# Kernel tuning notes

Measured on AMD Instinct MI355X. Metric: run time of the kernel, lower is better.

Reference implementation:

```python
import jax, jax.numpy as jnp
import numpy as np

B, L, D, H, NH, NL = 256, 201, 1536, 64, 2, 2
FF = 4 * H  # gnn hidden = hidden_units*4, ffn hidden = 4*d_model


def setup_inputs() -> dict:
    key = jax.random.key(0)
    ks = jax.random.split(key, 16)
    def nrm(k, shp, s=0.02):
        return jax.random.normal(k, shp, jnp.float32) * s
    return dict(
        interaction_list=jax.random.normal(ks[0], (B, L, D), jnp.float32),
        neg_list=jax.random.normal(ks[1], (B, L, D), jnp.float32),
        fc_w=nrm(ks[2], (D, H)), fc_b=jnp.zeros((H,), jnp.float32),
        mlp_w=nrm(ks[3], (H, H)), mlp_b=jnp.zeros((H,), jnp.float32),
        pos_emb=nrm(ks[4], (L, H)),
        ln0_g=jnp.ones((H,), jnp.float32), ln0_b=jnp.zeros((H,), jnp.float32),
        wqkv=nrm(ks[5], (NL, H, 3 * H)), bqkv=jnp.zeros((NL, 3 * H), jnp.float32),
        wo=nrm(ks[6], (NL, H, H)), bo=jnp.zeros((NL, H), jnp.float32),
        ln1_g=jnp.ones((NL, H), jnp.float32), ln1_b=jnp.zeros((NL, H), jnp.float32),
        w1=nrm(ks[7], (NL, H, FF)), b1=jnp.zeros((NL, FF), jnp.float32),
        w2=nrm(ks[8], (NL, FF, H)), b2=jnp.zeros((NL, H), jnp.float32),
        ln2_g=jnp.ones((NL, H), jnp.float32), ln2_b=jnp.zeros((NL, H), jnp.float32),
        wg1=nrm(ks[9], (D, FF)), bg1=jnp.zeros((FF,), jnp.float32),
        wg2=nrm(ks[10], (FF, H)), bg2=jnp.zeros((H,), jnp.float32),
        interaction_mask=jax.random.randint(ks[11], (B, L), 0, 2, jnp.int32),
    )


def _ln(x, g, b, eps=1e-5):
    m = x.mean(-1, keepdims=True)
    v = ((x - m) ** 2).mean(-1, keepdims=True)
    return (x - m) / jnp.sqrt(v + eps) * g + b


def _mlp_fc(x, fc_w, fc_b, mlp_w, mlp_b):
    # MLP_Layers: Linear(LLM_size->h) then dnn_layer x [Linear(h,h)+GELU]
    x = x @ fc_w + fc_b
    return jax.nn.gelu(x @ mlp_w + mlp_b)


def _user_encoder(x, mask_f, pos_emb, ln0_g, ln0_b, wqkv, bqkv, wo, bo,
                  ln1_g, ln1_b, w1, b1, w2, b2, ln2_g, ln2_b):
    b, l, h = x.shape
    dh = h // NH
    # causal AND key-valid attention bias: tril of (log_mask != 0) over keys
    causal = jnp.tril(jnp.ones((l, l), jnp.float32))  # [L,L]
    allowed = causal[None, :, :] * mask_f[:, None, :]  # [B,L,L]
    bias = jnp.where(allowed > 0, 0.0, -1e9).astype(x.dtype)
    x = _ln(x + pos_emb[None, :l, :], ln0_g, ln0_b)
    for i in range(NL):
        qkv = x @ wqkv[i] + bqkv[i]
        q, k, v = jnp.split(qkv, 3, axis=-1)
        q = q.reshape(b, l, NH, dh)
        k = k.reshape(b, l, NH, dh)
        v = v.reshape(b, l, NH, dh)
        scores = jnp.einsum('blhd,bmhd->bhlm', q, k) / jnp.sqrt(jnp.float32(dh))
        scores = scores + bias[:, None, :, :]
        attn = jax.nn.softmax(scores, axis=-1)
        o = jnp.einsum('bhlm,bmhd->blhd', attn, v).reshape(b, l, h)
        x = _ln(x + o @ wo[i] + bo[i], ln1_g[i], ln1_b[i])
        f = jax.nn.gelu(x @ w1[i] + b1[i]) @ w2[i] + b2[i]
        x = _ln(x + f, ln2_g[i], ln2_b[i])
    return x


def _forward(interaction_list, neg_list, fc_w, fc_b, mlp_w, mlp_b, pos_emb,
             ln0_g, ln0_b, wqkv, bqkv, wo, bo, ln1_g, ln1_b, w1, b1, w2, b2,
             ln2_g, ln2_b, wg1, bg1, wg2, bg2, interaction_mask):
    mask_f = interaction_mask.astype(jnp.float32)  # log_mask
    input_embs_all = _mlp_fc(interaction_list, fc_w, fc_b, mlp_w, mlp_b)  # [B,L,H]
    target_pos_embs = input_embs_all[:, 1:, :]
    target_neg_embs = _mlp_fc(neg_list, fc_w, fc_b, mlp_w, mlp_b)[:, :-1, :]
    # fused adjacency build: masked outer product + row normalize
    outer = mask_f[:, :, None] * mask_f[:, None, :]  # [B,L,L]
    row_sum = outer.sum(-1, keepdims=True)
    adj = outer / jnp.where(row_sum == 0, 1.0, row_sum)
    # 2-layer GCN on LLM embeddings: adj @ (x W)
    h1 = jax.nn.relu(jnp.einsum('blm,bmf->blf', adj, interaction_list @ wg1) + bg1)
    gnn_vec = jnp.einsum('blm,bmf->blf', adj, h1 @ wg2) + bg2  # [B,L,H]
    # cosine similarity (torch eps=1e-8), mean over seq then batch
    num = (input_embs_all * gnn_vec).sum(-1)
    na = jnp.maximum(jnp.linalg.norm(input_embs_all, axis=-1), 1e-8)
    nb = jnp.maximum(jnp.linalg.norm(gnn_vec, axis=-1), 1e-8)
    similarity = ((num / (na * nb)).sum(1) / input_embs_all.shape[1]).mean()
    prec_vec = _user_encoder(input_embs_all, mask_f, pos_emb, ln0_g, ln0_b,
                             wqkv, bqkv, wo, bo, ln1_g, ln1_b, w1, b1, w2, b2,
                             ln2_g, ln2_b)
    return (prec_vec[:, :-1, :], target_pos_embs, target_neg_embs,
            jnp.concatenate((input_embs_all, prec_vec), axis=2), similarity)


def reference(interaction_list, neg_list, fc_w, fc_b, mlp_w, mlp_b, pos_emb,
              ln0_g, ln0_b, wqkv, bqkv, wo, bo, ln1_g, ln1_b, w1, b1, w2, b2,
              ln2_g, ln2_b, wg1, bg1, wg2, bg2, interaction_mask):
    return _forward(interaction_list, neg_list, fc_w, fc_b, mlp_w, mlp_b,
                    pos_emb, ln0_g, ln0_b, wqkv, bqkv, wo, bo, ln1_g, ln1_b,
                    w1, b1, w2, b2, ln2_g, ln2_b, wg1, bg1, wg2, bg2,
                    interaction_mask)
```

## Files before the change

### kernel.cpp

```cpp
#include <hip/hip_runtime.h>
#include <math.h>

#define Bc 256
#define Lc 201
#define Dc 1536
#define Hc 64
#define DHc 32
#define FFc 256
#define Nc (Bc*Lc)

static constexpr size_t OFF1 = (size_t)Bc*(Lc-1)*Hc;
static constexpr size_t OFF2 = 2*OFF1;
static constexpr size_t OFF3 = 3*OFF1;
static constexpr size_t OFFS = OFF3 + (size_t)Bc*Lc*2*Hc;

__device__ __forceinline__ float wsum(float v){
  #pragma unroll
  for(int o=32;o>0;o>>=1) v += __shfl_xor(v,o,64);
  return v;
}
__device__ __forceinline__ float wmaxr(float v){
  #pragma unroll
  for(int o=32;o>0;o>>=1) v = fmaxf(v, __shfl_xor(v,o,64));
  return v;
}
__device__ __forceinline__ float gelu_t(float x){
  float x3 = x*x*x;
  return 0.5f*x*(1.f + tanhf(0.7978845608028654f*(x + 0.044715f*x3)));
}

#define DOT4(ACC,A,B) ACC = fmaf((A).x,(B).x, fmaf((A).y,(B).y, fmaf((A).z,(B).z, fmaf((A).w,(B).w,(ACC)))))
#define TILE16(ACC) \
  DOT4(ACC[0][0],a0,b0); DOT4(ACC[0][1],a0,b1); DOT4(ACC[0][2],a0,b2); DOT4(ACC[0][3],a0,b3); \
  DOT4(ACC[1][0],a1,b0); DOT4(ACC[1][1],a1,b1); DOT4(ACC[1][2],a1,b2); DOT4(ACC[1][3],a1,b3); \
  DOT4(ACC[2][0],a2,b0); DOT4(ACC[2][1],a2,b1); DOT4(ACC[2][2],a2,b2); DOT4(ACC[2][3],a2,b3); \
  DOT4(ACC[3][0],a3,b0); DOT4(ACC[3][1],a3,b1); DOT4(ACC[3][2],a3,b2); DOT4(ACC[3][3],a3,b3)

__global__ __launch_bounds__(256) void k_prep(
    const float* __restrict__ fcw, const float* __restrict__ wqkv,
    const float* __restrict__ wo,  const float* __restrict__ mw,
    const float* __restrict__ w1,  const float* __restrict__ w2,
    float* __restrict__ fwT, float* __restrict__ wqT, float* __restrict__ woT,
    float* __restrict__ mwT, float* __restrict__ w1T, float* __restrict__ w2T){
  int b = blockIdx.x, tid = threadIdx.x;
  if(b < 384){
    int c = b/6, k = (b - 6*(b/6))*256 + tid;
    fwT[(size_t)c*Dc + k] = fcw[(size_t)k*Hc + c];
  } else if(b < 480){
    int idx = (b-384)*256 + tid;
    int i = idx/12288, rem = idx - i*12288;
    int c = rem>>6, k = rem&63;
    wqT[(size_t)i*12288 + c*64 + k] = wqkv[(size_t)i*12288 + k*192 + c];
  } else if(b < 512){
    int idx = (b-480)*256 + tid;
    int i = idx>>12, rem = idx&4095;
    int c = rem>>6, k = rem&63;
    woT[(size_t)i*4096 + c*64 + k] = wo[(size_t)i*4096 + k*64 + c];
  } else if(b < 528){
    int idx = (b-512)*256 + tid;
    int c = idx>>6, k = idx&63;
    mwT[(size_t)c*64 + k] = mw[(size_t)k*64 + c];
  } else if(b < 656){
    int idx = (b-528)*256 + tid;
    int i = idx>>14, rem = idx&16383;
    int f = rem>>6, k = rem&63;
    w1T[(size_t)i*16384 + f*64 + k] = w1[(size_t)i*16384 + k*256 + f];
  } else {
    int idx = (b-656)*256 + tid;
    int i = idx>>14, rem = idx&16383;
    int h = rem>>8, f = rem&255;
    w2T[(size_t)i*16384 + h*256 + f] = w2[(size_t)i*16384 + f*64 + h];
  }
}

__global__ __launch_bounds__(256) void k_xsum(const float* __restrict__ X,
    const int* __restrict__ mask, float* __restrict__ xsum,
    float* __restrict__ Sb, float* __restrict__ simp){
  int b = blockIdx.x, tid = threadIdx.x;
  __shared__ float mk[Lc];
  for(int l = tid; l < Lc; l += 256) mk[l] = (float)mask[b*Lc + l];
  if(b==0 && tid==0) simp[0] = 0.f;
  __syncthreads();
  if(tid==0){ float s=0.f; for(int l=0;l<Lc;l++) s+=mk[l]; Sb[b]=s; }
  float acc[6];
  #pragma unroll
  for(int j=0;j<6;j++) acc[j]=0.f;
  const float* Xb = X + (size_t)b*Lc*Dc;
  for(int l=0;l<Lc;l++){
    if(mk[l] != 0.f){
      const float* row = Xb + (size_t)l*Dc;
      #pragma unroll
      for(int j=0;j<6;j++) acc[j] += row[j*256 + tid];
    }
  }
  #pragma unroll
  for(int j=0;j<6;j++) xsum[(size_t)b*Dc + j*256 + tid] = acc[j];
}

template<int MODE>
__global__ __launch_bounds__(256) void k_mlpfc(const float* __restrict__ X,
    const float* __restrict__ fwT, const float* __restrict__ fcb,
    const float* __restrict__ mwT, const float* __restrict__ mb,
    float* __restrict__ dst){
  __shared__ __align__(16) float xs[64][36];
  __shared__ __align__(16) float wts[64][36];
  __shared__ __align__(16) float yt[64][68];
  int tid = threadIdx.x;
  int n0 = blockIdx.x*64;
  int tr = tid>>4, tc = tid&15;
  float acc[4][4];
  #pragma unroll
  for(int i=0;i<4;i++){
    #pragma unroll
    for(int j=0;j<4;j++) acc[i][j]=0.f;
  }
  for(int k0=0;k0<Dc;k0+=32){
    #pragma unroll
    for(int i=0;i<8;i++){
      int idx = i*256+tid;
      int r = idx>>5, k = idx&31;
      xs[r][k]  = X[(size_t)(n0+r)*Dc + k0 + k];
      wts[r][k] = fwT[(size_t)r*Dc + k0 + k];
    }
    __syncthreads();
    #pragma unroll 4
    for(int k=0;k<32;k+=4){
      float4 a0=*(const float4*)&xs[tr   ][k];
      float4 a1=*(const float4*)&xs[tr+16][k];
      float4 a2=*(const float4*)&xs[tr+32][k];
      float4 a3=*(const float4*)&xs[tr+48][k];
      float4 b0=*(const float4*)&wts[tc   ][k];
      float4 b1=*(const float4*)&wts[tc+16][k];
      float4 b2=*(const float4*)&wts[tc+32][k];
      float4 b3=*(const float4*)&wts[tc+48][k];
      TILE16(acc);
    }
    __syncthreads();
  }
  #pragma unroll
  for(int i=0;i<4;i++){
    #pragma unroll
    for(int j=0;j<4;j++)
      yt[tr+16*i][tc+16*j] = acc[i][j] + fcb[tc+16*j];
  }
  __syncthreads();
  float acc2[4][4];
  #pragma unroll
  for(int i=0;i<4;i++){
    #pragma unroll
    for(int j=0;j<4;j++) acc2[i][j]=0.f;
  }
  #pragma unroll 4
  for(int k=0;k<64;k+=4){
    float4 a0=*(const float4*)&yt[tr   ][k];
    float4 a1=*(const float4*)&yt[tr+16][k];
    float4 a2=*(const float4*)&yt[tr+32][k];
    float4 a3=*(const float4*)&yt[tr+48][k];
    float4 b0=*(const float4*)&mwT[(size_t)(tc   )*64 + k];
    float4 b1=*(const float4*)&mwT[(size_t)(tc+16)*64 + k];
    float4 b2=*(const float4*)&mwT[(size_t)(tc+32)*64 + k];
    float4 b3=*(const float4*)&mwT[(size_t)(tc+48)*64 + k];
    TILE16(acc2);
  }
  #pragma unroll
  for(int i=0;i<4;i++){
    #pragma unroll
    for(int j=0;j<4;j++){
      int r = tr+16*i, c = tc+16*j;
      float v = gelu_t(acc2[i][j] + mb[c]);
      int n = n0 + r;
      if(MODE==0){
        dst[(size_t)n*Hc + c] = v;
      } else {
        int bb = n/Lc, l = n - bb*Lc;
        if(l < Lc-1) dst[((size_t)bb*(Lc-1) + l)*Hc + c] = v;
      }
    }
  }
}

__global__ __launch_bounds__(256) void k_gnn(const float* __restrict__ xsum,
    const float* __restrict__ Sb, const float* __restrict__ wg1,
    const float* __restrict__ bg1, const float* __restrict__ wg2,
    float* __restrict__ gvec){
  int b = blockIdx.x, tid = threadIdx.x;
  __shared__ float mx[Dc];
  __shared__ float h1s[FFc];
  float s = Sb[b];
  float inv = (s > 0.f) ? 1.f/s : 0.f;
  for(int i=tid;i<Dc;i+=256) mx[i] = xsum[(size_t)b*Dc+i]*inv;
  __syncthreads();
  float acc = 0.f;
  #pragma unroll 8
  for(int d=0;d<Dc;d++) acc += mx[d]*wg1[(size_t)d*FFc + tid];
  h1s[tid] = fmaxf(acc + bg1[tid], 0.f);
  __syncthreads();
  if(tid < Hc){
    float g = 0.f;
    #pragma unroll 8
    for(int f=0;f<FFc;f++) g += h1s[f]*wg2[f*Hc + tid];
    gvec[b*Hc + tid] = g;
  }
}

__global__ __launch_bounds__(256) void k_sim(const float* __restrict__ emb,
    const float* __restrict__ gvec, const float* __restrict__ bg2,
    const int* __restrict__ mask, float* __restrict__ simp){
  int b = blockIdx.x, tid = threadIdx.x;
  int wave = tid >> 6, lane = tid & 63;
  float gv_on = gvec[b*Hc + lane] + bg2[lane];
  float gv_off = bg2[lane];
  float accum = 0.f;
  for(int l = wave; l < Lc; l += 4){
    float e = emb[((size_t)b*Lc + l)*Hc + lane];
    float gv = (mask[b*Lc + l] != 0) ? gv_on : gv_off;
    float num = e*gv, na2 = e*e, nb2 = gv*gv;
    #pragma unroll
    for(int o=32;o>0;o>>=1){
      num += __shfl_xor(num,o,64);
      na2 += __shfl_xor(na2,o,64);
      nb2 += __shfl_xor(nb2,o,64);
    }
    if(lane==0){
      float na = fmaxf(sqrtf(na2),1e-8f), nb = fmaxf(sqrtf(nb2),1e-8f);
      accum += num/(na*nb);
    }
  }
  __shared__ float part[4];
  if(lane==0) part[wave]=accum;
  __syncthreads();
  if(tid==0){
    float t = part[0]+part[1]+part[2]+part[3];
    atomicAdd(simp, t * (1.0f/((float)Lc*(float)Bc)));
  }
}

__global__ __launch_bounds__(256) void k_ln0(const float* __restrict__ emb,
    const float* __restrict__ pos, const float* __restrict__ g,
    const float* __restrict__ be, float* __restrict__ x){
  int n = blockIdx.x*4 + (threadIdx.x>>6);
  int lane = threadIdx.x & 63;
  int l = n % Lc;
  float v = emb[(size_t)n*Hc + lane] + pos[l*Hc + lane];
  float m = wsum(v)*(1.f/64.f);
  float dv = v - m;
  float var = wsum(dv*dv)*(1.f/64.f);
  float r = rsqrtf(var + 1e-5f);
  x[(size_t)n*Hc + lane] = dv*r*g[lane] + be[lane];
}

__global__ __launch_bounds__(256) void k_qkv(const float* __restrict__ x,
    const float* __restrict__ wqT, const float* __restrict__ bias,
    float* __restrict__ qkv){
  __shared__ __align__(16) float xs[64][68];
  __shared__ __align__(16) float wt[64][68];
  int tid=threadIdx.x, n0=blockIdx.x*64, c0=blockIdx.y*64;
  #pragma unroll
  for(int i=0;i<16;i++){
    int idx=i*256+tid; int r=idx>>6, c=idx&63;
    xs[r][c]=x[(size_t)(n0+r)*Hc+c];
    wt[r][c]=wqT[(size_t)(c0+r)*64 + c];
  }
  __syncthreads();
  int tr=tid>>4, tc=tid&15;
  float acc[4][4];
  #pragma unroll
  for(int i=0;i<4;i++){
    #pragma unroll
    for(int j=0;j<4;j++) acc[i][j]=0.f;
  }
  #pragma unroll 4
  for(int k=0;k<64;k+=4){
    float4 a0=*(const float4*)&xs[tr   ][k];
    float4 a1=*(const float4*)&xs[tr+16][k];
    float4 a2=*(const float4*)&xs[tr+32][k];
    float4 a3=*(const float4*)&xs[tr+48][k];
    float4 b0=*(const float4*)&wt[tc   ][k];
    float4 b1=*(const float4*)&wt[tc+16][k];
    float4 b2=*(const float4*)&wt[tc+32][k];
    float4 b3=*(const float4*)&wt[tc+48][k];
    TILE16(acc);
  }
  #pragma unroll
  for(int i=0;i<4;i++){
    #pragma unroll
    for(int j=0;j<4;j++){
      int r=tr+16*i, c=tc+16*j;
      qkv[(size_t)(n0+r)*(3*Hc) + c0 + c] = acc[i][j] + bias[c0+c];
    }
  }
}

__global__ __launch_bounds__(256) void k_attn(const float* __restrict__ qkv,
    const int* __restrict__ mask, float* __restrict__ o){
  int b = blockIdx.x, h = blockIdx.y;
  int tid = threadIdx.x;
  __shared__ float kT[DHc][Lc];
  __shared__ float v_s[204][DHc];
  __shared__ float p_s[4][204];
  __shared__ float mkf[Lc];
  size_t base = (size_t)b*Lc;
  int qoff = h*DHc, koff = Hc + h*DHc, voff = 2*Hc + h*DHc;
  for(int idx = tid; idx < Lc*DHc; idx += 256){
    int l = idx >> 5, d = idx & 31;
    const float* row = qkv + (base + l)*(3*Hc);
    kT[d][l] = row[koff + d];
    v_s[l][d] = row[voff + d];
  }
  if(tid < 96) v_s[201 + (tid>>5)][tid&31] = 0.f;
  if(tid < 12) p_s[tid&3][201 + (tid>>2)] = 0.f;
  for(int idx = tid; idx < Lc; idx += 256) mkf[idx] = (float)mask[base + idx];
  __syncthreads();
  int wave = tid >> 6, lane = tid & 63;
  const float scale = 0.17677669529663687f;
  for(int it = 0; it < 51; it++){
    int l = it*4 + wave;
    if(l < Lc){
      float qv[DHc];
      const float* qrow = qkv + (base + l)*(3*Hc) + qoff;
      #pragma unroll
      for(int d=0;d<DHc;d++) qv[d] = qrow[d];
      float e[4]; float smax = -INFINITY;
      #pragma unroll
      for(int j=0;j<4;j++){
        int m = j*64 + lane;
        float s = -INFINITY;
        if(m < Lc){
          float dot = 0.f;
          #pragma unroll
          for(int d=0; d<DHc; d++) dot += qv[d]*kT[d][m];
          s = dot*scale;
          if(!((m <= l) && (mkf[m] != 0.f))) s -= 1e9f;
        }
        e[j] = s;
        smax = fmaxf(smax, s);
      }
      smax = wmaxr(smax);
      float ssum = 0.f;
      #pragma unroll
      for(int j=0;j<4;j++){
        int m = j*64 + lane;
        float ev = (m < Lc) ? expf(e[j] - smax) : 0.f;
        e[j] = ev; ssum += ev;
      }
      ssum = wsum(ssum);
      float inv = 1.f/ssum;
      #pragma unroll
      for(int j=0;j<4;j++){
        int m = j*64 + lane;
        if(m < Lc) p_s[wave][m] = e[j]*inv;
      }
      int d = lane & 31, hh = lane >> 5;
      float oacc = 0.f;
      const float* pr = &p_s[wave][0];
      #pragma unroll 4
      for(int t=0; t<102; t++){
        int m = 2*t + hh;
        oacc = fmaf(pr[m], v_s[m][d], oacc);
      }
      oacc += __shfl_xor(oacc, 32, 64);
      if(lane < DHc) o[(base + l)*Hc + h*DHc + lane] = oacc;
    }
  }
}

__global__ __launch_bounds__(256) void k_oln(const float* __restrict__ o,
    const float* __restrict__ woT, const float* __restrict__ bo,
    const float* __restrict__ g, const float* __restrict__ be,
    float* __restrict__ x){
  __shared__ __align__(16) float os[64][68];
  __shared__ __align__(16) float wt[64][68];
  __shared__ __align__(16) float yt[64][68];
  int tid=threadIdx.x, n0=blockIdx.x*64;
  #pragma unroll
  for(int i=0;i<16;i++){
    int idx=i*256+tid; int r=idx>>6, c=idx&63;
    os[r][c]=o[(size_t)(n0+r)*Hc+c];
    wt[r][c]=woT[(size_t)r*64+c];
  }
  __syncthreads();
  int tr=tid>>4, tc=tid&15;
  float acc[4][4];
  #pragma unroll
  for(int i=0;i<4;i++){
    #pragma unroll
    for(int j=0;j<4;j++) acc[i][j]=0.f;
  }
  #pragma unroll 4
  for(int k=0;k<64;k+=4){
    float4 a0=*(const float4*)&os[tr   ][k];
    float4 a1=*(const float4*)&os[tr+16][k];
    float4 a2=*(const float4*)&os[tr+32][k];
    float4 a3=*(const float4*)&os[tr+48][k];
    float4 b0=*(const float4*)&wt[tc   ][k];
    float4 b1=*(const float4*)&wt[tc+16][k];
    float4 b2=*(const float4*)&wt[tc+32][k];
    float4 b3=*(const float4*)&wt[tc+48][k];
    TILE16(acc);
  }
  #pragma unroll
  for(int i=0;i<4;i++){
    #pragma unroll
    for(int j=0;j<4;j++){
      int r=tr+16*i, c=tc+16*j;
      yt[r][c] = acc[i][j] + bo[c] + x[(size_t)(n0+r)*Hc+c];
    }
  }
  __syncthreads();
  int wave=tid>>6, lane=tid&63;
  for(int r=wave;r<64;r+=4){
    float v = yt[r][lane];
    float m = wsum(v)*(1.f/64.f);
    float dv = v - m;
    float var = wsum(dv*dv)*(1.f/64.f);
    float rr = rsqrtf(var + 1e-5f);
    x[(size_t)(n0+r)*Hc + lane] = dv*rr*g[lane] + be[lane];
  }
}

__global__ __launch_bounds__(256) void k_ffn(const float* __restrict__ xin,
    const float* __restrict__ w1T, const float* __restrict__ b1,
    const float* __restrict__ w2T, const float* __restrict__ b2,
    const float* __restrict__ g, const float* __restrict__ be,
    float* __restrict__ x){
  __shared__ __align__(16) float xs[64][68];
  __shared__ __align__(16) float wa[64][68];
  __shared__ __align__(16) float wb[64][68];
  __shared__ __align__(16) float ts[64][68];
  int tid=threadIdx.x, n0=blockIdx.x*64;
  int tr=tid>>4, tc=tid&15;
  #pragma unroll
  for(int i=0;i<16;i++){
    int idx=i*256+tid; int r=idx>>6, c=idx&63;
    xs[r][c]=xin[(size_t)(n0+r)*Hc+c];
  }
  float acc2[4][4];
  #pragma unroll
  for(int i=0;i<4;i++){
    #pragma unroll
    for(int j=0;j<4;j++) acc2[i][j]=0.f;
  }
  for(int cb=0; cb<4; cb++){
    int f0 = cb*64;
    __syncthreads();
    #pragma unroll
    for(int i=0;i<16;i++){
      int idx=i*256+tid; int r=idx>>6, c=idx&63;
      wa[r][c] = w1T[(size_t)(f0+r)*64 + c];
      wb[r][c] = w2T[(size_t)r*FFc + f0 + c];
    }
    __syncthreads();
    float acc1[4][4];
    #pragma unroll
    for(int i=0;i<4;i++){
      #pragma unroll
      for(int j=0;j<4;j++) acc1[i][j]=0.f;
    }
    #pragma unroll 4
    for(int k=0;k<64;k+=4){
      float4 a0=*(const float4*)&xs[tr   ][k];
      float4 a1=*(const float4*)&xs[tr+16][k];
      float4 a2=*(const float4*)&xs[tr+32][k];
      float4 a3=*(const float4*)&xs[tr+48][k];
      float4 b0=*(const float4*)&wa[tc   ][k];
      float4 b1=*(const float4*)&wa[tc+16][k];
      float4 b2=*(const float4*)&wa[tc+32][k];
      float4 b3=*(const float4*)&wa[tc+48][k];
      TILE16(acc1);
    }
    #pragma unroll
    for(int i=0;i<4;i++){
      #pragma unroll
      for(int j=0;j<4;j++)
        ts[tr+16*i][tc+16*j] = gelu_t(acc1[i][j] + b1[f0 + tc+16*j]);
    }
    __syncthreads();
    #pragma unroll 4
    for(int f=0;f<64;f+=4){
      float4 a0=*(const float4*)&ts[tr   ][f];
      float4 a1=*(const float4*)&ts[tr+16][f];
      float4 a2=*(const float4*)&ts[tr+32][f];
      float4 a3=*(const float4*)&ts[tr+48][f];
      float4 b0=*(const float4*)&wb[tc   ][f];
      float4 b1=*(const float4*)&wb[tc+16][f];
      float4 b2=*(const float4*)&wb[tc+32][f];
      float4 b3=*(const float4*)&wb[tc+48][f];
      TILE16(acc2);
    }
  }
  __syncthreads();
  #pragma unroll
  for(int i=0;i<4;i++){
    #pragma unroll
    for(int j=0;j<4;j++){
      int r=tr+16*i, c=tc+16*j;
      wa[r][c] = acc2[i][j] + b2[c] + xs[r][c];
    }
  }
  __syncthreads();
  int wave=tid>>6, lane=tid&63;
  for(int r=wave;r<64;r+=4){
    float v = wa[r][lane];
    float m = wsum(v)*(1.f/64.f);
    float dv = v - m;
    float var = wsum(dv*dv)*(1.f/64.f);
    float rr = rsqrtf(var + 1e-5f);
    x[(size_t)(n0+r)*Hc + lane] = dv*rr*g[lane] + be[lane];
  }
}

__global__ __launch_bounds__(256) void k_assemble(const float* __restrict__ emb,
    const float* __restrict__ xf, const float* __restrict__ simp,
    float* __restrict__ out){
  size_t idx = (size_t)blockIdx.x*256 + threadIdx.x;
  int h = (int)(idx & 63);
  size_t n = idx >> 6;
  int b = (int)(n / Lc);
  int l = (int)(n - (size_t)b*Lc);
  float e = emb[idx], p = xf[idx];
  out[OFF3 + n*128 + h] = e;
  out[OFF3 + n*128 + 64 + h] = p;
  if(l >= 1)   out[OFF1 + (((size_t)b*(Lc-1) + (l-1))<<6) + h] = e;
  if(l < Lc-1) out[(((size_t)b*(Lc-1) + l)<<6) + h] = p;
  if(idx == 0) out[OFFS] = simp[0];
}

extern "C" void kernel_launch(void* const* d_in, const int* in_sizes, int n_in,
                              void* d_out, int out_size, void* d_ws, size_t ws_size,
                              hipStream_t stream){
  (void)in_sizes; (void)n_in; (void)out_size; (void)ws_size;
  const float* X   = (const float*)d_in[0];
  const float* neg = (const float*)d_in[1];
  const float* fcw = (const float*)d_in[2];
  const float* fcb = (const float*)d_in[3];
  const float* mw  = (const float*)d_in[4];
  const float* mb  = (const float*)d_in[5];
  const float* pos = (const float*)d_in[6];
  const float* ln0g= (const float*)d_in[7];
  const float* ln0b= (const float*)d_in[8];
  const float* wqkv= (const float*)d_in[9];
  const float* bqkv= (const float*)d_in[10];
  const float* wo  = (const float*)d_in[11];
  const float* bo  = (const float*)d_in[12];
  const float* ln1g= (const float*)d_in[13];
  const float* ln1b= (const float*)d_in[14];
  const float* w1  = (const float*)d_in[15];
  const float* b1  = (const float*)d_in[16];
  const float* w2  = (const float*)d_in[17];
  const float* b2  = (const float*)d_in[18];
  const float* ln2g= (const float*)d_in[19];
  const float* ln2b= (const float*)d_in[20];
  const float* wg1 = (const float*)d_in[21];
  const float* bg1 = (const float*)d_in[22];
  const float* wg2 = (const float*)d_in[23];
  const float* bg2 = (const float*)d_in[24];
  const int*   msk = (const int*)d_in[25];
  float* out = (float*)d_out;

  float* ws   = (float*)d_ws;
  float* emb  = ws;
  float* x    = emb  + (size_t)Nc*Hc;
  float* oatt = x    + (size_t)Nc*Hc;
  float* qkv  = oatt + (size_t)Nc*Hc;
  float* xsum = qkv  + (size_t)Nc*3*Hc;
  float* Sb   = xsum + (size_t)Bc*Dc;
  float* gvec = Sb   + Bc;
  float* wqT  = gvec + (size_t)Bc*Hc;
  float* woT  = wqT  + 24576;
  float* w1T  = woT  + 8192;
  float* w2T  = w1T  + 32768;
  float* simp = w2T  + 32768;
  float* fwT  = qkv;
  float* mwT  = qkv + (size_t)Hc*Dc;

  k_prep<<<784,256,0,stream>>>(fcw, wqkv, wo, mw, w1, w2,
                               fwT, wqT, woT, mwT, w1T, w2T);
  k_xsum<<<Bc,256,0,stream>>>(X, msk, xsum, Sb, simp);
  k_mlpfc<0><<<Nc/64,256,0,stream>>>(X, fwT, fcb, mwT, mb, emb);
  k_mlpfc<1><<<Nc/64,256,0,stream>>>(neg, fwT, fcb, mwT, mb, out + OFF2);
  k_gnn<<<Bc,256,0,stream>>>(xsum, Sb, wg1, bg1, wg2, gvec);
  k_sim<<<Bc,256,0,stream>>>(emb, gvec, bg2, msk, simp);
  k_ln0<<<Nc/4,256,0,stream>>>(emb, pos, ln0g, ln0b, x);
  for(int i=0;i<2;i++){
    k_qkv<<<dim3(Nc/64,3),256,0,stream>>>(x, wqT + (size_t)i*12288, bqkv + i*3*Hc, qkv);
    k_attn<<<dim3(Bc,2),256,0,stream>>>(qkv, msk, oatt);
    k_oln<<<Nc/64,256,0,stream>>>(oatt, woT + (size_t)i*4096, bo + i*Hc,
                                  ln1g + i*Hc, ln1b + i*Hc, x);
    k_ffn<<<Nc/64,256,0,stream>>>(x, w1T + (size_t)i*16384, b1 + i*FFc,
                                  w2T + (size_t)i*16384, b2 + i*Hc,
                                  ln2g + i*Hc, ln2b + i*Hc, x);
  }
  k_assemble<<<(Nc*Hc)/256,256,0,stream>>>(emb, x, simp, out);
}
```

Measured before the change: 1.994 ms.

## Restructure MLP-FC and FFN GEMMs to wave-uniform weight reads with transposed LDS activations

The FC/MLP and FFN kernels now give each wave 16 output columns and each lane one row. Activations are transposed into LDS, and weights are read directly from global memory in their original layout with wave-uniform addresses, so the weight-transpose prep work is dropped. The FC kernel double-buffers the X tile with register prefetch, xsum is split across 6 column blocks for more parallelism, and GELU uses an exp/rcp sigmoid form. The risk is lower per-thread reuse (1x16 tile instead of 4x4) and heavier scalar or global weight traffic, with a slight change in GELU accuracy.

```diff
diff --git a/kernel.cpp b/kernel.cpp
--- a/kernel.cpp
+++ b/kernel.cpp
@@ -24,157 +24,140 @@
   for(int o=32;o>0;o>>=1) v = fmaxf(v, __shfl_xor(v,o,64));
   return v;
 }
-__device__ __forceinline__ float gelu_t(float x){
-  float x3 = x*x*x;
-  return 0.5f*x*(1.f + tanhf(0.7978845608028654f*(x + 0.044715f*x3)));
-}
-
-#define DOT4(ACC,A,B) ACC = fmaf((A).x,(B).x, fmaf((A).y,(B).y, fmaf((A).z,(B).z, fmaf((A).w,(B).w,(ACC)))))
-#define TILE16(ACC) \
-  DOT4(ACC[0][0],a0,b0); DOT4(ACC[0][1],a0,b1); DOT4(ACC[0][2],a0,b2); DOT4(ACC[0][3],a0,b3); \
-  DOT4(ACC[1][0],a1,b0); DOT4(ACC[1][1],a1,b1); DOT4(ACC[1][2],a1,b2); DOT4(ACC[1][3],a1,b3); \
-  DOT4(ACC[2][0],a2,b0); DOT4(ACC[2][1],a2,b1); DOT4(ACC[2][2],a2,b2); DOT4(ACC[2][3],a2,b3); \
-  DOT4(ACC[3][0],a3,b0); DOT4(ACC[3][1],a3,b1); DOT4(ACC[3][2],a3,b2); DOT4(ACC[3][3],a3,b3)
+__device__ __forceinline__ float gelu_f(float x){
+  float t2 = 1.5957691216057308f*(x + 0.044715f*x*x*x);
+  float e = __expf(-t2);
+  return x * __builtin_amdgcn_rcpf(1.f + e);
+}
 
 __global__ __launch_bounds__(256) void k_prep(
-    const float* __restrict__ fcw, const float* __restrict__ wqkv,
-    const float* __restrict__ wo,  const float* __restrict__ mw,
-    const float* __restrict__ w1,  const float* __restrict__ w2,
-    float* __restrict__ fwT, float* __restrict__ wqT, float* __restrict__ woT,
-    float* __restrict__ mwT, float* __restrict__ w1T, float* __restrict__ w2T){
+    const float* __restrict__ wqkv, const float* __restrict__ wo,
+    float* __restrict__ wqT, float* __restrict__ woT){
   int b = blockIdx.x, tid = threadIdx.x;
-  if(b < 384){
-    int c = b/6, k = (b - 6*(b/6))*256 + tid;
-    fwT[(size_t)c*Dc + k] = fcw[(size_t)k*Hc + c];
-  } else if(b < 480){
-    int idx = (b-384)*256 + tid;
+  if(b < 96){
+    int idx = b*256 + tid;
     int i = idx/12288, rem = idx - i*12288;
     int c = rem>>6, k = rem&63;
     wqT[(size_t)i*12288 + c*64 + k] = wqkv[(size_t)i*12288 + k*192 + c];
-  } else if(b < 512){
-    int idx = (b-480)*256 + tid;
+  } else {
+    int idx = (b-96)*256 + tid;
     int i = idx>>12, rem = idx&4095;
     int c = rem>>6, k = rem&63;
     woT[(size_t)i*4096 + c*64 + k] = wo[(size_t)i*4096 + k*64 + c];
-  } else if(b < 528){
-    int idx = (b-512)*256 + tid;
-    int c = idx>>6, k = idx&63;
-    mwT[(size_t)c*64 + k] = mw[(size_t)k*64 + c];
-  } else if(b < 656){
-    int idx = (b-528)*256 + tid;
-    int i = idx>>14, rem = idx&16383;
-    int f = rem>>6, k = rem&63;
-    w1T[(size_t)i*16384 + f*64 + k] = w1[(size_t)i*16384 + k*256 + f];
-  } else {
-    int idx = (b-656)*256 + tid;
-    int i = idx>>14, rem = idx&16383;
-    int h = rem>>8, f = rem&255;
-    w2T[(size_t)i*16384 + h*256 + f] = w2[(size_t)i*16384 + f*64 + h];
   }
 }
 
 __global__ __launch_bounds__(256) void k_xsum(const float* __restrict__ X,
     const int* __restrict__ mask, float* __restrict__ xsum,
     float* __restrict__ Sb, float* __restrict__ simp){
-  int b = blockIdx.x, tid = threadIdx.x;
+  int j = blockIdx.x, b = blockIdx.y, tid = threadIdx.x;
   __shared__ float mk[Lc];
   for(int l = tid; l < Lc; l += 256) mk[l] = (float)mask[b*Lc + l];
-  if(b==0 && tid==0) simp[0] = 0.f;
-  __syncthreads();
-  if(tid==0){ float s=0.f; for(int l=0;l<Lc;l++) s+=mk[l]; Sb[b]=s; }
-  float acc[6];
-  #pragma unroll
-  for(int j=0;j<6;j++) acc[j]=0.f;
-  const float* Xb = X + (size_t)b*Lc*Dc;
+  if(j==0 && b==0 && tid==0) simp[0] = 0.f;
+  __syncthreads();
+  if(j==0 && tid==0){ float s=0.f; for(int l=0;l<Lc;l++) s+=mk[l]; Sb[b]=s; }
+  float acc = 0.f;
+  const float* Xb = X + (size_t)b*Lc*Dc + j*256 + tid;
   for(int l=0;l<Lc;l++){
-    if(mk[l] != 0.f){
-      const float* row = Xb + (size_t)l*Dc;
-      #pragma unroll
-      for(int j=0;j<6;j++) acc[j] += row[j*256 + tid];
-    }
-  }
-  #pragma unroll
-  for(int j=0;j<6;j++) xsum[(size_t)b*Dc + j*256 + tid] = acc[j];
+    if(mk[l] != 0.f) acc += Xb[(size_t)l*Dc];
+  }
+  xsum[(size_t)b*Dc + j*256 + tid] = acc;
 }
 
 template<int MODE>
 __global__ __launch_bounds__(256) void k_mlpfc(const float* __restrict__ X,
-    const float* __restrict__ fwT, const float* __restrict__ fcb,
-    const float* __restrict__ mwT, const float* __restrict__ mb,
+    const float* __restrict__ fcw, const float* __restrict__ fcb,
+    const float* __restrict__ mw, const float* __restrict__ mb,
     float* __restrict__ dst){
-  __shared__ __align__(16) float xs[64][36];
-  __shared__ __align__(16) float wts[64][36];
-  __shared__ __align__(16) float yt[64][68];
-  int tid = threadIdx.x;
+  __shared__ float SM[2*64*68 + 64*66];
+  float* xsT = SM;
+  float* ytT = SM + 2*64*68;
+  int tid = threadIdx.x, lane = tid & 63;
+  int w = __builtin_amdgcn_readfirstlane(tid >> 6);
+  int c0 = 16*w;
   int n0 = blockIdx.x*64;
-  int tr = tid>>4, tc = tid&15;
-  float acc[4][4];
-  #pragma unroll
-  for(int i=0;i<4;i++){
-    #pragma unroll
-    for(int j=0;j<4;j++) acc[i][j]=0.f;
-  }
-  for(int k0=0;k0<Dc;k0+=32){
-    #pragma unroll
-    for(int i=0;i<8;i++){
-      int idx = i*256+tid;
-      int r = idx>>5, k = idx&31;
-      xs[r][k]  = X[(size_t)(n0+r)*Dc + k0 + k];
-      wts[r][k] = fwT[(size_t)r*Dc + k0 + k];
+  int sr = tid >> 2, sa = tid & 3;
+  const float* Xst = X + (size_t)(n0 + sr)*Dc + 4*sa;
+  float4 v0 = *(const float4*)(Xst);
+  float4 v1 = *(const float4*)(Xst + 16);
+  float4 v2 = *(const float4*)(Xst + 32);
+  float4 v3 = *(const float4*)(Xst + 48);
+  {
+    float* d = xsT + 4*sa*68 + sr;
+    d[0]=v0.x; d[68]=v0.y; d[136]=v0.z; d[204]=v0.w; d += 16*68;
+    d[0]=v1.x; d[68]=v1.y; d[136]=v1.z; d[204]=v1.w; d += 16*68;
+    d[0]=v2.x; d[68]=v2.y; d[136]=v2.z; d[204]=v2.w; d += 16*68;
+    d[0]=v3.x; d[68]=v3.y; d[136]=v3.z; d[204]=v3.w;
+  }
+  float acc[16];
+  #pragma unroll
+  for(int j=0;j<16;j++) acc[j]=0.f;
+  __syncthreads();
+  for(int t=0;t<24;t++){
+    if(t<23){
+      const float* q = Xst + (t+1)*64;
+      v0 = *(const float4*)(q);
+      v1 = *(const float4*)(q+16);
+      v2 = *(const float4*)(q+32);
+      v3 = *(const float4*)(q+48);
+    }
+    const float* cur = xsT + (t&1)*(64*68) + lane;
+    const float* wp = fcw + (size_t)t*64*64 + c0;
+    #pragma unroll 8
+    for(int k=0;k<64;k++){
+      float av = cur[k*68];
+      const float* wk = wp + (size_t)k*64;
+      #pragma unroll
+      for(int j=0;j<16;j++) acc[j] = fmaf(av, wk[j], acc[j]);
+    }
+    if(t<23){
+      float* d = xsT + ((t+1)&1)*(64*68) + 4*sa*68 + sr;
+      d[0]=v0.x; d[68]=v0.y; d[136]=v0.z; d[204]=v0.w; d += 16*68;
+      d[0]=v1.x; d[68]=v1.y; d[136]=v1.z; d[204]=v1.w; d += 16*68;
+      d[0]=v2.x; d[68]=v2.y; d[136]=v2.z; d[204]=v2.w; d += 16*68;
+      d[0]=v3.x; d[68]=v3.y; d[136]=v3.z; d[204]=v3.w;
     }
     __syncthreads();
-    #pragma unroll 4
-    for(int k=0;k<32;k+=4){
-      float4 a0=*(const float4*)&xs[tr   ][k];
-      float4 a1=*(const float4*)&xs[tr+16][k];
-      float4 a2=*(const float4*)&xs[tr+32][k];
-      float4 a3=*(const float4*)&xs[tr+48][k];
-      float4 b0=*(const float4*)&wts[tc   ][k];
-      float4 b1=*(const float4*)&wts[tc+16][k];
-      float4 b2=*(const float4*)&wts[tc+32][k];
-      float4 b3=*(const float4*)&wts[tc+48][k];
-      TILE16(acc);
-    }
-    __syncthreads();
-  }
-  #pragma unroll
-  for(int i=0;i<4;i++){
-    #pragma unroll
-    for(int j=0;j<4;j++)
-      yt[tr+16*i][tc+16*j] = acc[i][j] + fcb[tc+16*j];
-  }
-  __syncthreads();
-  float acc2[4][4];
-  #pragma unroll
-  for(int i=0;i<4;i++){
-    #pragma unroll
-    for(int j=0;j<4;j++) acc2[i][j]=0.f;
-  }
-  #pragma unroll 4
-  for(int k=0;k<64;k+=4){
-    float4 a0=*(const float4*)&yt[tr   ][k];
-    float4 a1=*(const float4*)&yt[tr+16][k];
-    float4 a2=*(const float4*)&yt[tr+32][k];
-    float4 a3=*(const float4*)&yt[tr+48][k];
-    float4 b0=*(const float4*)&mwT[(size_t)(tc   )*64 + k];
-    float4 b1=*(const float4*)&mwT[(size_t)(tc+16)*64 + k];
-    float4 b2=*(const float4*)&mwT[(size_t)(tc+32)*64 + k];
-    float4 b3=*(const float4*)&mwT[(size_t)(tc+48)*64 + k];
-    TILE16(acc2);
-  }
-  #pragma unroll
-  for(int i=0;i<4;i++){
-    #pragma unroll
-    for(int j=0;j<4;j++){
-      int r = tr+16*i, c = tc+16*j;
-      float v = gelu_t(acc2[i][j] + mb[c]);
-      int n = n0 + r;
-      if(MODE==0){
-        dst[(size_t)n*Hc + c] = v;
-      } else {
-        int bb = n/Lc, l = n - bb*Lc;
-        if(l < Lc-1) dst[((size_t)bb*(Lc-1) + l)*Hc + c] = v;
-      }
+  }
+  #pragma unroll
+  for(int j=0;j<16;j++) ytT[(c0+j)*66 + lane] = acc[j] + fcb[c0+j];
+  __syncthreads();
+  float acc2[16];
+  #pragma unroll
+  for(int j=0;j<16;j++) acc2[j]=0.f;
+  {
+    const float* yb = ytT + lane;
+    const float* wp2 = mw + c0;
+    #pragma unroll 8
+    for(int c=0;c<64;c++){
+      float av = yb[c*66];
+      const float* wk = wp2 + (size_t)c*64;
+      #pragma unroll
+      for(int j=0;j<16;j++) acc2[j] = fmaf(av, wk[j], acc2[j]);
+    }
+  }
+  float* g_s = SM;
+  #pragma unroll
+  for(int q=0;q<4;q++){
+    float4 gv;
+    gv.x = gelu_f(acc2[4*q+0] + mb[c0+4*q+0]);
+    gv.y = gelu_f(acc2[4*q+1] + mb[c0+4*q+1]);
+    gv.z = gelu_f(acc2[4*q+2] + mb[c0+4*q+2]);
+    gv.w = gelu_f(acc2[4*q+3] + mb[c0+4*q+3]);
+    *(float4*)&g_s[lane*68 + c0 + 4*q] = gv;
+  }
+  __syncthreads();
+  #pragma unroll
+  for(int p=0;p<4;p++){
+    int idx = p*256 + tid;
+    int rr = idx>>4, q = idx&15;
+    float4 gv = *(const float4*)&g_s[rr*68 + 4*q];
+    int n = n0 + rr;
+    if(MODE==0){
+      *(float4*)&dst[(size_t)n*Hc + 4*q] = gv;
+    } else {
+      int bb = n/Lc, l = n - bb*Lc;
+      if(l < Lc-1) *(float4*)&dst[((size_t)bb*(Lc-1) + l)*Hc + 4*q] = gv;
     }
   }
 }
@@ -279,7 +262,11 @@
     float4 b1=*(const float4*)&wt[tc+16][k];
     float4 b2=*(const float4*)&wt[tc+32][k];
     float4 b3=*(const float4*)&wt[tc+48][k];
-    TILE16(acc);
+    #define DOT4(ACC,A,B) ACC = fmaf((A).x,(B).x, fmaf((A).y,(B).y, fmaf((A).z,(B).z, fmaf((A).w,(B).w,(ACC)))))
+    DOT4(acc[0][0],a0,b0); DOT4(acc[0][1],a0,b1); DOT4(acc[0][2],a0,b2); DOT4(acc[0][3],a0,b3);
+    DOT4(acc[1][0],a1,b0); DOT4(acc[1][1],a1,b1); DOT4(acc[1][2],a1,b2); DOT4(acc[1][3],a1,b3);
+    DOT4(acc[2][0],a2,b0); DOT4(acc[2][1],a2,b1); DOT4(acc[2][2],a2,b2); DOT4(acc[2][3],a2,b3);
+    DOT4(acc[3][0],a3,b0); DOT4(acc[3][1],a3,b1); DOT4(acc[3][2],a3,b2); DOT4(acc[3][3],a3,b3);
   }
   #pragma unroll
   for(int i=0;i<4;i++){
@@ -396,7 +383,10 @@
     float4 b1=*(const float4*)&wt[tc+16][k];
     float4 b2=*(const float4*)&wt[tc+32][k];
     float4 b3=*(const float4*)&wt[tc+48][k];
-    TILE16(acc);
+    DOT4(acc[0][0],a0,b0); DOT4(acc[0][1],a0,b1); DOT4(acc[0][2],a0,b2); DOT4(acc[0][3],a0,b3);
+    DOT4(acc[1][0],a1,b0); DOT4(acc[1][1],a1,b1); DOT4(acc[1][2],a1,b2); DOT4(acc[1][3],a1,b3);
+    DOT4(acc[2][0],a2,b0); DOT4(acc[2][1],a2,b1); DOT4(acc[2][2],a2,b2); DOT4(acc[2][3],a2,b3);
+    DOT4(acc[3][0],a3,b0); DOT4(acc[3][1],a3,b1); DOT4(acc[3][2],a3,b2); DOT4(acc[3][3],a3,b3);
   }
   #pragma unroll
   for(int i=0;i<4;i++){
@@ -419,93 +409,83 @@
 }
 
 __global__ __launch_bounds__(256) void k_ffn(const float* __restrict__ xin,
-    const float* __restrict__ w1T, const float* __restrict__ b1,
-    const float* __restrict__ w2T, const float* __restrict__ b2,
+    const float* __restrict__ w1, const float* __restrict__ b1,
+    const float* __restrict__ w2, const float* __restrict__ b2,
     const float* __restrict__ g, const float* __restrict__ be,
     float* __restrict__ x){
-  __shared__ __align__(16) float xs[64][68];
-  __shared__ __align__(16) float wa[64][68];
-  __shared__ __align__(16) float wb[64][68];
-  __shared__ __align__(16) float ts[64][68];
-  int tid=threadIdx.x, n0=blockIdx.x*64;
-  int tr=tid>>4, tc=tid&15;
+  __shared__ float SM[64*68 + 64*66];
+  float* xT = SM;
+  float* tsT = SM + 64*68;
+  int tid = threadIdx.x, lane = tid & 63;
+  int w = __builtin_amdgcn_readfirstlane(tid >> 6);
+  int c0 = 16*w;
+  int n0 = blockIdx.x*64;
+  int sr = tid >> 2, sa = tid & 3;
+  {
+    const float* q = xin + (size_t)(n0+sr)*Hc + 4*sa;
+    float4 v0 = *(const float4*)(q);
+    float4 v1 = *(const float4*)(q+16);
+    float4 v2 = *(const float4*)(q+32);
+    float4 v3 = *(const float4*)(q+48);
+    float* d = xT + 4*sa*68 + sr;
+    d[0]=v0.x; d[68]=v0.y; d[136]=v0.z; d[204]=v0.w; d += 16*68;
+    d[0]=v1.x; d[68]=v1.y; d[136]=v1.z; d[204]=v1.w; d += 16*68;
+    d[0]=v2.x; d[68]=v2.y; d[136]=v2.z; d[204]=v2.w; d += 16*68;
+    d[0]=v3.x; d[68]=v3.y; d[136]=v3.z; d[204]=v3.w;
+  }
+  float acc2[16];
+  #pragma unroll
+  for(int j=0;j<16;j++) acc2[j]=0.f;
+  __syncthreads();
+  for(int p=0;p<4;p++){
+    float acc1[16];
+    #pragma unroll
+    for(int j=0;j<16;j++) acc1[j]=0.f;
+    const float* xb = xT + lane;
+    const float* wp1 = w1 + p*64 + c0;
+    #pragma unroll 8
+    for(int k=0;k<64;k++){
+      float av = xb[k*68];
+      const float* wk = wp1 + (size_t)k*FFc;
+      #pragma unroll
+      for(int j=0;j<16;j++) acc1[j] = fmaf(av, wk[j], acc1[j]);
+    }
+    __syncthreads();
+    #pragma unroll
+    for(int j=0;j<16;j++)
+      tsT[(c0+j)*66 + lane] = gelu_f(acc1[j] + b1[p*64 + c0 + j]);
+    __syncthreads();
+    const float* tb = tsT + lane;
+    const float* wp2 = w2 + (size_t)p*64*64 + c0;
+    #pragma unroll 8
+    for(int f=0;f<64;f++){
+      float av = tb[f*66];
+      const float* wk = wp2 + (size_t)f*64;
+      #pragma unroll
+      for(int j=0;j<16;j++) acc2[j] = fmaf(av, wk[j], acc2[j]);
+    }
+  }
+  float vres[16];
+  #pragma unroll
+  for(int j=0;j<16;j++) vres[j] = acc2[j] + b2[c0+j] + xT[(c0+j)*68 + lane];
+  __syncthreads();
+  float* g_s = SM;
+  #pragma unroll
+  for(int q=0;q<4;q++){
+    float4 gv;
+    gv.x = vres[4*q+0]; gv.y = vres[4*q+1]; gv.z = vres[4*q+2]; gv.w = vres[4*q+3];
+    *(float4*)&g_s[lane*68 + c0 + 4*q] = gv;
+  }
+  __syncthreads();
   #pragma unroll
   for(int i=0;i<16;i++){
-    int idx=i*256+tid; int r=idx>>6, c=idx&63;
-    xs[r][c]=xin[(size_t)(n0+r)*Hc+c];
-  }
-  float acc2[4][4];
-  #pragma unroll
-  for(int i=0;i<4;i++){
-    #pragma unroll
-    for(int j=0;j<4;j++) acc2[i][j]=0.f;
-  }
-  for(int cb=0; cb<4; cb++){
-    int f0 = cb*64;
-    __syncthreads();
-    #pragma unroll
-    for(int i=0;i<16;i++){
-      int idx=i*256+tid; int r=idx>>6, c=idx&63;
-      wa[r][c] = w1T[(size_t)(f0+r)*64 + c];
-      wb[r][c] = w2T[(size_t)r*FFc + f0 + c];
-    }
-    __syncthreads();
-    float acc1[4][4];
-    #pragma unroll
-    for(int i=0;i<4;i++){
-      #pragma unroll
-      for(int j=0;j<4;j++) acc1[i][j]=0.f;
-    }
-    #pragma unroll 4
-    for(int k=0;k<64;k+=4){
-      float4 a0=*(const float4*)&xs[tr   ][k];
-      float4 a1=*(const float4*)&xs[tr+16][k];
-      float4 a2=*(const float4*)&xs[tr+32][k];
-      float4 a3=*(const float4*)&xs[tr+48][k];
-      float4 b0=*(const float4*)&wa[tc   ][k];
-      float4 b1=*(const float4*)&wa[tc+16][k];
-      float4 b2=*(const float4*)&wa[tc+32][k];
-      float4 b3=*(const float4*)&wa[tc+48][k];
-      TILE16(acc1);
-    }
-    #pragma unroll
-    for(int i=0;i<4;i++){
-      #pragma unroll
-      for(int j=0;j<4;j++)
-        ts[tr+16*i][tc+16*j] = gelu_t(acc1[i][j] + b1[f0 + tc+16*j]);
-    }
-    __syncthreads();
-    #pragma unroll 4
-    for(int f=0;f<64;f+=4){
-      float4 a0=*(const float4*)&ts[tr   ][f];
-      float4 a1=*(const float4*)&ts[tr+16][f];
-      float4 a2=*(const float4*)&ts[tr+32][f];
-      float4 a3=*(const float4*)&ts[tr+48][f];
-      float4 b0=*(const float4*)&wb[tc   ][f];
-      float4 b1=*(const float4*)&wb[tc+16][f];
-      float4 b2=*(const float4*)&wb[tc+32][f];
-      float4 b3=*(const float4*)&wb[tc+48][f];
-      TILE16(acc2);
-    }
-  }
-  __syncthreads();
-  #pragma unroll
-  for(int i=0;i<4;i++){
-    #pragma unroll
-    for(int j=0;j<4;j++){
-      int r=tr+16*i, c=tc+16*j;
-      wa[r][c] = acc2[i][j] + b2[c] + xs[r][c];
-    }
-  }
-  __syncthreads();
-  int wave=tid>>6, lane=tid&63;
-  for(int r=wave;r<64;r+=4){
-    float v = wa[r][lane];
+    int rr = 16*w + i;
+    float v = g_s[rr*68 + lane];
     float m = wsum(v)*(1.f/64.f);
     float dv = v - m;
     float var = wsum(dv*dv)*(1.f/64.f);
-    float rr = rsqrtf(var + 1e-5f);
-    x[(size_t)(n0+r)*Hc + lane] = dv*rr*g[lane] + be[lane];
+    float rq = rsqrtf(var + 1e-5f);
+    x[(size_t)(n0+rr)*Hc + lane] = dv*rq*g[lane] + be[lane];
   }
 }
 
@@ -567,17 +547,12 @@
   float* gvec = Sb   + Bc;
   float* wqT  = gvec + (size_t)Bc*Hc;
   float* woT  = wqT  + 24576;
-  float* w1T  = woT  + 8192;
-  float* w2T  = w1T  + 32768;
-  float* simp = w2T  + 32768;
-  float* fwT  = qkv;
-  float* mwT  = qkv + (size_t)Hc*Dc;
-
-  k_prep<<<784,256,0,stream>>>(fcw, wqkv, wo, mw, w1, w2,
-                               fwT, wqT, woT, mwT, w1T, w2T);
-  k_xsum<<<Bc,256,0,stream>>>(X, msk, xsum, Sb, simp);
-  k_mlpfc<0><<<Nc/64,256,0,stream>>>(X, fwT, fcb, mwT, mb, emb);
-  k_mlpfc<1><<<Nc/64,256,0,stream>>>(neg, fwT, fcb, mwT, mb, out + OFF2);
+  float* simp = woT  + 8192;
+
+  k_prep<<<128,256,0,stream>>>(wqkv, wo, wqT, woT);
+  k_xsum<<<dim3(6,Bc),256,0,stream>>>(X, msk, xsum, Sb, simp);
+  k_mlpfc<0><<<Nc/64,256,0,stream>>>(X, fcw, fcb, mw, mb, emb);
+  k_mlpfc<1><<<Nc/64,256,0,stream>>>(neg, fcw, fcb, mw, mb, out + OFF2);
   k_gnn<<<Bc,256,0,stream>>>(xsum, Sb, wg1, bg1, wg2, gvec);
   k_sim<<<Bc,256,0,stream>>>(emb, gvec, bg2, msk, simp);
   k_ln0<<<Nc/4,256,0,stream>>>(emb, pos, ln0g, ln0b, x);
@@ -586,8 +561,8 @@
     k_attn<<<dim3(Bc,2),256,0,stream>>>(qkv, msk, oatt);
     k_oln<<<Nc/64,256,0,stream>>>(oatt, woT + (size_t)i*4096, bo + i*Hc,
                                   ln1g + i*Hc, ln1b + i*Hc, x);
-    k_ffn<<<Nc/64,256,0,stream>>>(x, w1T + (size_t)i*16384, b1 + i*FFc,
-                                  w2T + (size_t)i*16384, b2 + i*Hc,
+    k_ffn<<<Nc/64,256,0,stream>>>(x, w1 + (size_t)i*Hc*FFc, b1 + i*FFc,
+                                  w2 + (size_t)i*FFc*Hc, b2 + i*Hc,
                                   ln2g + i*Hc, ln2b + i*Hc, x);
   }
   k_assemble<<<(Nc*Hc)/256,256,0,stream>>>(emb, x, simp, out);
```

Measured after the change: 2.009 ms. About the same (+0.8%).
